# Optimization experiments

Hardware: AMD Instinct MI355X
Metric: run time of the kernel (lower is better)

Reference implementation:

```python
import jax, jax.numpy as jnp
import numpy as np

EPS = 1e-12  # layer_norm_eps

def _ln(h, g, b):
    m = jnp.mean(h, axis=-1, keepdims=True)
    v = jnp.var(h, axis=-1, keepdims=True)
    return (h - m) / jnp.sqrt(v + EPS) * g + b

def setup_inputs() -> dict:
    key = jax.random.key(0)
    B, L, C, N = 32, 512, 256, 16
    ks = jax.random.split(key, 8)
    f = jax.random.normal
    return {
        'query': f(ks[0], (B, L, C), jnp.float32),
        'x': f(ks[1], (B, L, C), jnp.float32),
        'offset': f(ks[2], (B, L, 2 * N), jnp.float32) * 0.1,
        'w1': f(ks[3], (L, L // 4), jnp.float32) * 0.02, 'b1': jnp.zeros((L // 4,), jnp.float32),
        'g1': jnp.ones((L // 4,), jnp.float32), 'bt1': jnp.zeros((L // 4,), jnp.float32),
        'w2': f(ks[4], (L // 4, L), jnp.float32) * 0.02, 'b2': jnp.zeros((L,), jnp.float32),
        'w3': f(ks[5], (C, C), jnp.float32) * 0.02, 'b3': jnp.zeros((C,), jnp.float32),
        'g3': jnp.ones((C,), jnp.float32), 'bt3': jnp.zeros((C,), jnp.float32),
        'w4': f(ks[6], (C, 2 * N), jnp.float32) * 0.02, 'b4': jnp.zeros((2 * N,), jnp.float32),
    }

def reference(query, x, offset, w1, b1, g1, bt1, w2, b2, w3, b3, g3, bt3, w4, b4):
    B, L, C = x.shape
    N = w4.shape[1] // 2
    # sample_layer: Linear over the sequence axis (query permuted to [B,C,L])
    q = jnp.swapaxes(query, 1, 2)                                        # [B,C,L]
    q = jax.nn.gelu(_ln(q @ w1 + b1, g1, bt1), approximate=False) @ w2 + b2
    q = jnp.swapaxes(q, 1, 2)                                            # [B,L,C]
    # adjust_layer over channels -> per-step 2N offsets, tanh * 0.02
    adj = jax.nn.gelu(_ln(q @ w3 + b3, g3, bt3), approximate=False) @ w4 + b4
    adj = jnp.tanh(adj) * 0.02                                           # [B,L,2N]
    local = (offset + adj).reshape(B, L, N, 2)
    # precomputed reference points (x-coord 0, y-coord depends on query step i)
    i = jnp.arange(L, dtype=x.dtype)
    n = jnp.arange(N, dtype=x.dtype) + 0.5
    ref_y = n[None, :] * 2.0 * (i[:, None] + 1e-9) / (N * L) - 1.0       # [L,N]
    ref = jnp.stack([jnp.zeros_like(ref_y), ref_y], axis=-1)             # [L,N,2]
    pos = jnp.tanh(local + ref[None])                                    # [B,L,N,2]
    # grid_sample equivalent: input [B*L, C, H=L, W=1], align_corners=True,
    # bilinear, zero padding. With W=1 the x-coordinate always maps to col 0,
    # so only pos[...,1] matters. Causal mask zeroes keys h > query step l
    # before sampling; since bilinear sampling is linear in the input, we mask
    # the two gathered taps instead of materializing the O(B*L*L*C) tensor.
    pix = (pos[..., 1] + 1.0) * 0.5 * (L - 1)                            # [B,L,N]
    i0f = jnp.floor(pix)
    frac = pix - i0f
    i0 = i0f.astype(jnp.int32)
    i1 = i0 + 1
    lpos = jnp.arange(L, dtype=jnp.int32)[None, :, None]
    v0 = (i0 >= 0) & (i0 < L) & (i0 <= lpos)
    v1 = (i1 >= 0) & (i1 < L) & (i1 <= lpos)
    c0 = jnp.clip(i0, 0, L - 1)
    c1 = jnp.clip(i1, 0, L - 1)
    bidx = jnp.arange(B)[:, None, None]
    val0 = x[bidx, c0]                                                   # [B,L,N,C]
    val1 = x[bidx, c1]                                                   # [B,L,N,C]
    w0 = jnp.where(v0, 1.0 - frac, 0.0)
    w1_ = jnp.where(v1, frac, 0.0)
    out = w0[..., None] * val0 + w1_[..., None] * val1                   # [B,L,N,C]
    return (out, offset, pos)
```

## Files before the change

kernel.cpp:

```cpp
#include <hip/hip_runtime.h>
#include <hip/hip_fp16.h>
#include <math.h>


typedef _Float16 f16;
typedef _Float16 f16x8 __attribute__((ext_vector_type(8)));
typedef float f32x4 __attribute__((ext_vector_type(4)));

#define ZERO4 f32x4{0.f, 0.f, 0.f, 0.f}

__device__ __forceinline__ float gelu_exact(float v) {
  return 0.5f * v * (1.0f + erff(v * 0.70710678118654752f));
}

__global__ __launch_bounds__(256) void k0_prep(
    const float* __restrict__ w1, const float* __restrict__ w2,
    const float* __restrict__ w3, const float* __restrict__ w4,
    f16* __restrict__ w1T, f16* __restrict__ w2T,
    f16* __restrict__ w3T, f16* __restrict__ w4T) {
  __shared__ f16 tile[64][80];
  int blk = blockIdx.x;
  const int tid = threadIdx.x;
  const float* in; f16* out; int R, Cc, tr, tc;
  if (blk < 16)      { in = w1; out = w1T; R = 512; Cc = 128; tr = blk >> 1; tc = blk & 1; }
  else if (blk < 32) { blk -= 16; in = w2; out = w2T; R = 128; Cc = 512; tr = blk >> 3; tc = blk & 7; }
  else if (blk < 48) { blk -= 32; in = w3; out = w3T; R = 256; Cc = 256; tr = blk >> 2; tc = blk & 3; }
  else               { blk -= 48; in = w4; out = w4T; R = 256; Cc = 32;  tr = blk;      tc = 0; }
  const int r0 = tr * 64, c0 = tc * 64;
  for (int id = tid; id < 4096; id += 256) {
    int rr = id >> 6, cc = id & 63;
    if (c0 + cc < Cc) tile[cc][rr] = (f16)in[(r0 + rr) * Cc + c0 + cc];
  }
  __syncthreads();
  for (int id = tid; id < 512; id += 256) {
    int cc = id >> 3, ch = id & 7;
    if (c0 + cc < Cc)
      *(f16x8*)(out + (c0 + cc) * R + r0 + ch * 8) = *(f16x8*)&tile[cc][ch * 8];
  }
}

__global__ __launch_bounds__(256) void k12_sample(
    const float* __restrict__ query, const f16* __restrict__ w1T,
    const f16* __restrict__ w2T,
    const float* __restrict__ b1, const float* __restrict__ g1,
    const float* __restrict__ bt1, const float* __restrict__ b2,
    f16* __restrict__ qout) {
  __shared__ char pool[38912];
  const int tid = threadIdx.x;
  const int b = blockIdx.x >> 4;
  const int c0 = (blockIdx.x & 15) << 4;
  const int lane = tid & 63, w = tid >> 6;
  const int mrow = lane & 15, kg = lane >> 4;
  char* At = pool;
  char* Bt = pool + 2048;
  char* t1s = pool + 32768;
  float* sb2 = (float*)(pool + 36864);

  sb2[tid] = b2[tid];
  sb2[tid + 256] = b2[tid + 256];

  const int qll = tid >> 4, qcc = tid & 15;
  const int wrj = tid >> 3, wch = tid & 7;
  float qv[4]; f16x8 wv[4];
#pragma unroll
  for (int it = 0; it < 4; ++it) {
    qv[it] = query[(((b << 9) + qll + it * 16) << 8) + c0 + qcc];
    wv[it] = *(const f16x8*)(w1T + (wrj + it * 32) * 512 + wch * 8);
  }

  f32x4 acc[2] = {ZERO4, ZERO4};
  for (int s = 0; s < 8; ++s) {
#pragma unroll
    for (int it = 0; it < 4; ++it) {
      int ll = qll + it * 16;
      *(f16*)(At + qcc * 128 + ((2 * ll) ^ ((qcc & 7) << 4))) = (f16)qv[it];
    }
#pragma unroll
    for (int it = 0; it < 4; ++it) {
      int rj = wrj + it * 32;
      *(f16x8*)(Bt + rj * 128 + ((wch * 16) ^ ((rj & 7) << 4))) = wv[it];
    }
    __syncthreads();
    if (s < 7) {
      const int k0n = (s + 1) << 6;
#pragma unroll
      for (int it = 0; it < 4; ++it) {
        qv[it] = query[(((b << 9) + k0n + qll + it * 16) << 8) + c0 + qcc];
        wv[it] = *(const f16x8*)(w1T + (wrj + it * 32) * 512 + k0n + wch * 8);
      }
    }
#pragma unroll
    for (int kk = 0; kk < 2; ++kk) {
      f16x8 a = *(const f16x8*)(At + mrow * 128 + (((kk << 6) + (kg << 4)) ^ ((mrow & 7) << 4)));
#pragma unroll
      for (int nf = 0; nf < 2; ++nf) {
        int rn = w * 32 + nf * 16 + mrow;
        f16x8 bfr = *(const f16x8*)(Bt + rn * 128 + (((kk << 6) + (kg << 4)) ^ ((rn & 7) << 4)));
        acc[nf] = __builtin_amdgcn_mfma_f32_16x16x32_f16(a, bfr, acc[nf], 0, 0, 0);
      }
    }
    __syncthreads();
  }

  f16x8 av[8];
#pragma unroll
  for (int it = 0; it < 8; ++it)
    av[it] = *(const f16x8*)(w2T + ((tid >> 4) + it * 16) * 128 + (tid & 15) * 8);

  float (*hs)[132] = (float(*)[132])pool;
#pragma unroll
  for (int nf = 0; nf < 2; ++nf)
#pragma unroll
    for (int i = 0; i < 4; ++i)
      hs[kg * 4 + i][w * 32 + nf * 16 + mrow] = acc[nf][i];
  __syncthreads();
  {
    const int r = tid >> 4, g = tid & 15;
    float s1 = 0.f, s2 = 0.f, vals[8];
#pragma unroll
    for (int jj = 0; jj < 8; ++jj) {
      int j = g * 8 + jj;
      float v = hs[r][j] + b1[j];
      vals[jj] = v; s1 += v; s2 += v * v;
    }
#pragma unroll
    for (int m = 1; m < 16; m <<= 1) { s1 += __shfl_xor(s1, m, 64); s2 += __shfl_xor(s2, m, 64); }
    const float mean = s1 * (1.f / 128.f);
    float var = fmaxf(s2 * (1.f / 128.f) - mean * mean, 0.f);
    const float rstd = rsqrtf(var + 1e-12f);
    f16 ov[8];
#pragma unroll
    for (int jj = 0; jj < 8; ++jj) {
      int j = g * 8 + jj;
      float v = (vals[jj] - mean) * rstd * g1[j] + bt1[j];
      ov[jj] = (f16)gelu_exact(v);
    }
    __syncthreads();
    *(f16x8*)(t1s + r * 256 + ((g * 16) ^ ((r & 7) << 4))) = *(f16x8*)ov;
  }
  __syncthreads();

  char* At2 = pool;
  const int ar2 = tid >> 4, ac2 = tid & 15;
  for (int lc = 0; lc < 4; ++lc) {
#pragma unroll
    for (int it = 0; it < 8; ++it) {
      int r = ar2 + it * 16;
      *(f16x8*)(At2 + r * 256 + ((ac2 * 16) ^ ((r & 7) << 4))) = av[it];
    }
    __syncthreads();
    if (lc < 3) {
#pragma unroll
      for (int it = 0; it < 8; ++it)
        av[it] = *(const f16x8*)(w2T + ((lc + 1) * 128 + ar2 + it * 16) * 128 + ac2 * 8);
    }
    f32x4 acc2[2] = {ZERO4, ZERO4};
#pragma unroll
    for (int ks = 0; ks < 4; ++ks) {
      f16x8 bfr = *(const f16x8*)(t1s + mrow * 256 + (((ks << 6) + (kg << 4)) ^ ((mrow & 7) << 4)));
#pragma unroll
      for (int mf = 0; mf < 2; ++mf) {
        int rm = w * 32 + mf * 16 + mrow;
        f16x8 a = *(const f16x8*)(At2 + rm * 256 + (((ks << 6) + (kg << 4)) ^ ((rm & 7) << 4)));
        acc2[mf] = __builtin_amdgcn_mfma_f32_16x16x32_f16(a, bfr, acc2[mf], 0, 0, 0);
      }
    }
#pragma unroll
    for (int mf = 0; mf < 2; ++mf)
#pragma unroll
      for (int i = 0; i < 4; ++i) {
        int l = lc * 128 + w * 32 + mf * 16 + kg * 4 + i;
        qout[((b << 9) + l) * 256 + c0 + mrow] = (f16)(acc2[mf][i] + sb2[l]);
      }
    __syncthreads();
  }
}

__global__ __launch_bounds__(256) void k3_adjust(
    const f16* __restrict__ qbuf, const f16* __restrict__ w3T,
    const float* __restrict__ b3, const float* __restrict__ g3,
    const float* __restrict__ bt3, const f16* __restrict__ w4T,
    const float* __restrict__ b4, const float* __restrict__ offset,
    float* __restrict__ off_out, float* __restrict__ pos_out) {
  __shared__ char pool[34816];
  __shared__ char w4t[32 * 512];
  __shared__ float sb3[256];
  const int tid = threadIdx.x;
  const int b = blockIdx.x >> 5;
  const int l0 = (blockIdx.x & 31) << 4;
  const int lane = tid & 63, w = tid >> 6;
  const int mrow = lane & 15, kg = lane >> 4;
  char* At = pool;
  char* Bt = pool + 2048;

  for (int id = tid; id < 1024; id += 256) {
    int r = id >> 5, c = id & 31;
    f16x8 v = *(const f16x8*)(w4T + r * 256 + c * 8);
    *(f16x8*)(w4t + r * 512 + ((c * 16) ^ ((r & 7) << 4))) = v;
  }
  sb3[tid] = b3[tid];

  const int sr = tid >> 3, sc = tid & 7;
  f16x8 aq; f16x8 bq[8];
  if (tid < 128) aq = *(const f16x8*)(qbuf + ((b << 9) + l0 + sr) * 256 + sc * 8);
#pragma unroll
  for (int it = 0; it < 8; ++it)
    bq[it] = *(const f16x8*)(w3T + (sr + it * 32) * 256 + sc * 8);

  f32x4 acc[4] = {ZERO4, ZERO4, ZERO4, ZERO4};
  for (int s = 0; s < 4; ++s) {
    if (tid < 128)
      *(f16x8*)(At + sr * 128 + ((sc * 16) ^ ((sr & 7) << 4))) = aq;
#pragma unroll
    for (int it = 0; it < 8; ++it) {
      int r = sr + it * 32;
      *(f16x8*)(Bt + r * 128 + ((sc * 16) ^ ((r & 7) << 4))) = bq[it];
    }
    __syncthreads();
    if (s < 3) {
      const int k0n = (s + 1) << 6;
      if (tid < 128) aq = *(const f16x8*)(qbuf + ((b << 9) + l0 + sr) * 256 + k0n + sc * 8);
#pragma unroll
      for (int it = 0; it < 8; ++it)
        bq[it] = *(const f16x8*)(w3T + (sr + it * 32) * 256 + k0n + sc * 8);
    }
#pragma unroll
    for (int kk = 0; kk < 2; ++kk) {
      f16x8 a = *(const f16x8*)(At + mrow * 128 + (((kk << 6) + (kg << 4)) ^ ((mrow & 7) << 4)));
#pragma unroll
      for (int nf = 0; nf < 4; ++nf) {
        int rn = w * 64 + nf * 16 + mrow;
        f16x8 bfr = *(const f16x8*)(Bt + rn * 128 + (((kk << 6) + (kg << 4)) ^ ((rn & 7) << 4)));
        acc[nf] = __builtin_amdgcn_mfma_f32_16x16x32_f16(a, bfr, acc[nf], 0, 0, 0);
      }
    }
    __syncthreads();
  }
  float (*hs)[264] = (float(*)[264])pool;
  char* ts = pool + 17408;
#pragma unroll
  for (int nf = 0; nf < 4; ++nf) {
    int col = w * 64 + nf * 16 + mrow;
    float bias = sb3[col];
#pragma unroll
    for (int i = 0; i < 4; ++i)
      hs[kg * 4 + i][col] = acc[nf][i] + bias;
  }
  __syncthreads();
  {
    const int r = tid >> 4, g = tid & 15;
    float s1 = 0.f, s2 = 0.f, vals[16];
#pragma unroll
    for (int jj = 0; jj < 16; ++jj) {
      float v = hs[r][g * 16 + jj];
      vals[jj] = v; s1 += v; s2 += v * v;
    }
#pragma unroll
    for (int m = 1; m < 16; m <<= 1) { s1 += __shfl_xor(s1, m, 64); s2 += __shfl_xor(s2, m, 64); }
    const float mean = s1 * (1.f / 256.f);
    float var = fmaxf(s2 * (1.f / 256.f) - mean * mean, 0.f);
    const float rstd = rsqrtf(var + 1e-12f);
    f16 ov[16];
#pragma unroll
    for (int jj = 0; jj < 16; ++jj) {
      int kch = g * 16 + jj;
      float v = (vals[jj] - mean) * rstd * g3[kch] + bt3[kch];
      ov[jj] = (f16)gelu_exact(v);
    }
    *(f16x8*)(ts + r * 512 + ((g * 32) ^ ((r & 7) << 4))) = *(f16x8*)&ov[0];
    *(f16x8*)(ts + r * 512 + ((g * 32 + 16) ^ ((r & 7) << 4))) = *(f16x8*)&ov[8];
  }
  __syncthreads();
  if (w < 2) {
    const int n4 = w;
    f32x4 a4 = ZERO4;
#pragma unroll
    for (int ks = 0; ks < 8; ++ks) {
      f16x8 a = *(const f16x8*)(ts + mrow * 512 + (((ks << 6) + (kg << 4)) ^ ((mrow & 7) << 4)));
      int br = n4 * 16 + mrow;
      f16x8 bb = *(const f16x8*)(w4t + br * 512 + (((ks << 6) + (kg << 4)) ^ ((br & 7) << 4)));
      a4 = __builtin_amdgcn_mfma_f32_16x16x32_f16(a, bb, a4, 0, 0, 0);
    }
    const int col = n4 * 16 + mrow;
#pragma unroll
    for (int i = 0; i < 4; ++i) {
      const int row = kg * 4 + i;
      const int l = l0 + row;
      float adj = tanhf(a4[i] + b4[col]) * 0.02f;
      float padj = __shfl_xor(adj, 1, 64);
      if ((lane & 1) == 0) {
        const int n = col >> 1;
        const float2 offv = *(const float2*)(offset + (((b << 9) + l) << 5) + col);
        const float pos0v = tanhf(offv.x + adj);
        const float ref_y = ((float)n + 0.5f) * ((float)l + 1e-9f) * (1.0f / 4096.0f) - 1.0f;
        const float pos1v = tanhf(offv.y + padj + ref_y);
        *(float2*)(off_out + (((b << 9) + l) << 5) + col) = offv;
        *(float2*)(pos_out + (((b << 9) + l) << 5) + col) = make_float2(pos0v, pos1v);
      }
    }
  }
}

__global__ __launch_bounds__(256) void k4_gather(
    const float* __restrict__ x, const float* __restrict__ pos,
    float* __restrict__ outbuf) {
  const int blk = blockIdx.x;
  const int b = ((blk & 7) << 2) | ((blk >> 3) & 3);
  const int grp = blk >> 5;
  const int w = threadIdx.x >> 6, lane = threadIdx.x & 63;
  const int p0 = (grp << 5) + (w << 3);
  const unsigned tbase = ((unsigned)b << 13) + (unsigned)p0;
  const f32x4* xb = (const f32x4*)x + ((unsigned)(b << 9)) * 64u + lane;
  f32x4* ob = (f32x4*)outbuf + (unsigned)tbase * 64u + lane;

  float pw[8];
#pragma unroll
  for (int i = 0; i < 8; ++i) pw[i] = pos[(tbase + i) * 2 + 1];

  int cc0[8], cc1[8];
  float w0v[8], w1v[8];
#pragma unroll
  for (int i = 0; i < 8; ++i) {
    const int l = (p0 + i) >> 4;
    const float pix = (pw[i] + 1.0f) * 0.5f * 511.0f;
    const float i0f = floorf(pix);
    const int i0 = (int)i0f;
    const float frac = pix - i0f;
    const int i1 = i0 + 1;
    const bool v0 = (i0 >= 0) && (i0 < 512) && (i0 <= l);
    const bool v1 = (i1 >= 0) && (i1 < 512) && (i1 <= l);
    cc0[i] = i0 < 0 ? 0 : (i0 > 511 ? 511 : i0);
    cc1[i] = i1 < 0 ? 0 : (i1 > 511 ? 511 : i1);
    w0v[i] = v0 ? (1.0f - frac) : 0.0f;
    w1v[i] = v1 ? frac : 0.0f;
  }

#pragma unroll
  for (int g = 0; g < 2; ++g) {
    f32x4 va[4], vb[4];
#pragma unroll
    for (int j = 0; j < 4; ++j) {
      va[j] = xb[(unsigned)cc0[g * 4 + j] * 64u];
      vb[j] = xb[(unsigned)cc1[g * 4 + j] * 64u];
    }
#pragma unroll
    for (int j = 0; j < 4; ++j) {
      f32x4 o = w0v[g * 4 + j] * va[j] + w1v[g * 4 + j] * vb[j];
      __builtin_nontemporal_store(o, ob + (unsigned)(g * 4 + j) * 64u);
    }
  }
}

extern "C" void kernel_launch(void* const* d_in, const int* in_sizes, int n_in,
                              void* d_out, int out_size, void* d_ws, size_t ws_size,
                              hipStream_t stream) {
  const float* query  = (const float*)d_in[0];
  const float* x      = (const float*)d_in[1];
  const float* offset = (const float*)d_in[2];
  const float* w1  = (const float*)d_in[3];
  const float* b1  = (const float*)d_in[4];
  const float* g1  = (const float*)d_in[5];
  const float* bt1 = (const float*)d_in[6];
  const float* w2  = (const float*)d_in[7];
  const float* b2  = (const float*)d_in[8];
  const float* w3  = (const float*)d_in[9];
  const float* b3  = (const float*)d_in[10];
  const float* g3  = (const float*)d_in[11];
  const float* bt3 = (const float*)d_in[12];
  const float* w4  = (const float*)d_in[13];
  const float* b4  = (const float*)d_in[14];

  float* out     = (float*)d_out;
  float* off_out = out + 67108864;
  float* pos_out = off_out + 524288;

  f16* w1T = (f16*)d_ws;
  f16* w2T = w1T + 65536;
  f16* w3T = w2T + 65536;
  f16* w4T = w3T + 65536;
  f16* q   = w4T + 8192;

  k0_prep<<<52, 256, 0, stream>>>(w1, w2, w3, w4, w1T, w2T, w3T, w4T);
  k12_sample<<<512, 256, 0, stream>>>(query, w1T, w2T, b1, g1, bt1, b2, q);
  k3_adjust<<<1024, 256, 0, stream>>>(q, w3T, b3, g3, bt3, w4T, b4, offset,
                                      off_out, pos_out);
  k4_gather<<<8192, 256, 0, stream>>>(x, pos_out, out);
}
```

Measured before the change: 109.1 us.

## Split fused sample kernel into split-K GEMM1, LayerNorm, and tiled GEMM2 kernels

Replaces the single fused sample-layer kernel with three kernels: a split-K first GEMM over four K-chunks writing fp32 partials (2048 blocks), a reduction+LayerNorm+GELU kernel producing an fp16 intermediate, and a larger-tile second GEMM with 64-column output tiles. The aim is more parallelism and better occupancy than the earlier 512-block serial-K fused kernel. It also drops the LDS staging of w4 and b3 in the adjust kernel, reading them directly from global memory. In exchange it adds global round trips for the partials and intermediate, plus two extra launches.

```diff
diff --git a/kernel.cpp b/kernel.cpp
--- a/kernel.cpp
+++ b/kernel.cpp
@@ -39,37 +39,32 @@
   }
 }
 
-__global__ __launch_bounds__(256) void k12_sample(
+__global__ __launch_bounds__(256) void k1_gemm1(
     const float* __restrict__ query, const f16* __restrict__ w1T,
-    const f16* __restrict__ w2T,
-    const float* __restrict__ b1, const float* __restrict__ g1,
-    const float* __restrict__ bt1, const float* __restrict__ b2,
-    f16* __restrict__ qout) {
-  __shared__ char pool[38912];
+    float* __restrict__ hpart) {
+  __shared__ __align__(16) char pool[18432];
   const int tid = threadIdx.x;
-  const int b = blockIdx.x >> 4;
-  const int c0 = (blockIdx.x & 15) << 4;
+  const int b = blockIdx.x >> 6;
+  const int c0 = ((blockIdx.x >> 2) & 15) << 4;
+  const int ks = blockIdx.x & 3;
   const int lane = tid & 63, w = tid >> 6;
   const int mrow = lane & 15, kg = lane >> 4;
   char* At = pool;
   char* Bt = pool + 2048;
-  char* t1s = pool + 32768;
-  float* sb2 = (float*)(pool + 36864);
-
-  sb2[tid] = b2[tid];
-  sb2[tid + 256] = b2[tid + 256];
 
   const int qll = tid >> 4, qcc = tid & 15;
   const int wrj = tid >> 3, wch = tid & 7;
+  const int kbase = ks << 7;
+
   float qv[4]; f16x8 wv[4];
 #pragma unroll
   for (int it = 0; it < 4; ++it) {
-    qv[it] = query[(((b << 9) + qll + it * 16) << 8) + c0 + qcc];
-    wv[it] = *(const f16x8*)(w1T + (wrj + it * 32) * 512 + wch * 8);
+    qv[it] = query[(((b << 9) + kbase + qll + it * 16) << 8) + c0 + qcc];
+    wv[it] = *(const f16x8*)(w1T + (wrj + it * 32) * 512 + kbase + wch * 8);
   }
 
   f32x4 acc[2] = {ZERO4, ZERO4};
-  for (int s = 0; s < 8; ++s) {
+  for (int s = 0; s < 2; ++s) {
 #pragma unroll
     for (int it = 0; it < 4; ++it) {
       int ll = qll + it * 16;
@@ -81,8 +76,8 @@
       *(f16x8*)(Bt + rj * 128 + ((wch * 16) ^ ((rj & 7) << 4))) = wv[it];
     }
     __syncthreads();
-    if (s < 7) {
-      const int k0n = (s + 1) << 6;
+    if (s == 0) {
+      const int k0n = kbase + 64;
 #pragma unroll
       for (int it = 0; it < 4; ++it) {
         qv[it] = query[(((b << 9) + k0n + qll + it * 16) << 8) + c0 + qcc];
@@ -101,79 +96,109 @@
     }
     __syncthreads();
   }
-
-  f16x8 av[8];
-#pragma unroll
-  for (int it = 0; it < 8; ++it)
-    av[it] = *(const f16x8*)(w2T + ((tid >> 4) + it * 16) * 128 + (tid & 15) * 8);
-
-  float (*hs)[132] = (float(*)[132])pool;
+  const unsigned hb = ((unsigned)ks << 20) + ((unsigned)b << 15);
 #pragma unroll
   for (int nf = 0; nf < 2; ++nf)
 #pragma unroll
     for (int i = 0; i < 4; ++i)
-      hs[kg * 4 + i][w * 32 + nf * 16 + mrow] = acc[nf][i];
+      hpart[hb + ((unsigned)(c0 + kg * 4 + i) << 7) + (unsigned)(w * 32 + nf * 16 + mrow)] = acc[nf][i];
+}
+
+__global__ __launch_bounds__(256) void k2a_ln(
+    const float* __restrict__ hpart, const float* __restrict__ b1,
+    const float* __restrict__ g1, const float* __restrict__ bt1,
+    f16* __restrict__ t1) {
+  const int tid = threadIdx.x;
+  const int row = blockIdx.x * 16 + (tid >> 4);
+  const int g = tid & 15;
+  const int j0 = g * 8;
+  const unsigned base = ((unsigned)row << 7) + (unsigned)j0;
+
+  float a8[8] = {0.f, 0.f, 0.f, 0.f, 0.f, 0.f, 0.f, 0.f};
+#pragma unroll
+  for (int ks = 0; ks < 4; ++ks) {
+    const float* p = hpart + ((unsigned)ks << 20) + base;
+    f32x4 u0 = *(const f32x4*)p;
+    f32x4 u1 = *(const f32x4*)(p + 4);
+    a8[0] += u0.x; a8[1] += u0.y; a8[2] += u0.z; a8[3] += u0.w;
+    a8[4] += u1.x; a8[5] += u1.y; a8[6] += u1.z; a8[7] += u1.w;
+  }
+  float vals[8], s1 = 0.f, s2 = 0.f;
+#pragma unroll
+  for (int jj = 0; jj < 8; ++jj) {
+    float v = a8[jj] + b1[j0 + jj];
+    vals[jj] = v; s1 += v; s2 += v * v;
+  }
+#pragma unroll
+  for (int m = 1; m < 16; m <<= 1) { s1 += __shfl_xor(s1, m, 64); s2 += __shfl_xor(s2, m, 64); }
+  const float mean = s1 * (1.f / 128.f);
+  float var = fmaxf(s2 * (1.f / 128.f) - mean * mean, 0.f);
+  const float rstd = rsqrtf(var + 1e-12f);
+  f16 ov[8];
+#pragma unroll
+  for (int jj = 0; jj < 8; ++jj) {
+    float v = (vals[jj] - mean) * rstd * g1[j0 + jj] + bt1[j0 + jj];
+    ov[jj] = (f16)gelu_exact(v);
+  }
+  *(f16x8*)(t1 + base) = *(f16x8*)ov;
+}
+
+__global__ __launch_bounds__(256) void k2b_gemm2(
+    const f16* __restrict__ w2T, const f16* __restrict__ t1,
+    const float* __restrict__ b2, f16* __restrict__ qout) {
+  __shared__ __align__(16) char pool[49152];
+  const int tid = threadIdx.x;
+  const int b = blockIdx.x >> 4;
+  const int l0 = ((blockIdx.x >> 2) & 3) << 7;
+  const int c0 = (blockIdx.x & 3) << 6;
+  const int lane = tid & 63, w = tid >> 6;
+  const int mrow = lane & 15, kg = lane >> 4;
+  char* At2 = pool;
+  char* Bt2 = pool + 32768;
+
+  const int r16 = tid >> 4, cch = tid & 15;
+#pragma unroll
+  for (int it = 0; it < 8; ++it) {
+    int r = r16 + it * 16;
+    f16x8 v = *(const f16x8*)(w2T + (l0 + r) * 128 + cch * 8);
+    *(f16x8*)(At2 + r * 256 + ((cch * 16) ^ ((r & 7) << 4))) = v;
+  }
+#pragma unroll
+  for (int it = 0; it < 4; ++it) {
+    int r = r16 + it * 16;
+    f16x8 v = *(const f16x8*)(t1 + ((b << 8) + c0 + r) * 128 + cch * 8);
+    *(f16x8*)(Bt2 + r * 256 + ((cch * 16) ^ ((r & 7) << 4))) = v;
+  }
   __syncthreads();
-  {
-    const int r = tid >> 4, g = tid & 15;
-    float s1 = 0.f, s2 = 0.f, vals[8];
-#pragma unroll
-    for (int jj = 0; jj < 8; ++jj) {
-      int j = g * 8 + jj;
-      float v = hs[r][j] + b1[j];
-      vals[jj] = v; s1 += v; s2 += v * v;
-    }
-#pragma unroll
-    for (int m = 1; m < 16; m <<= 1) { s1 += __shfl_xor(s1, m, 64); s2 += __shfl_xor(s2, m, 64); }
-    const float mean = s1 * (1.f / 128.f);
-    float var = fmaxf(s2 * (1.f / 128.f) - mean * mean, 0.f);
-    const float rstd = rsqrtf(var + 1e-12f);
-    f16 ov[8];
-#pragma unroll
-    for (int jj = 0; jj < 8; ++jj) {
-      int j = g * 8 + jj;
-      float v = (vals[jj] - mean) * rstd * g1[j] + bt1[j];
-      ov[jj] = (f16)gelu_exact(v);
-    }
-    __syncthreads();
-    *(f16x8*)(t1s + r * 256 + ((g * 16) ^ ((r & 7) << 4))) = *(f16x8*)ov;
-  }
-  __syncthreads();
-
-  char* At2 = pool;
-  const int ar2 = tid >> 4, ac2 = tid & 15;
-  for (int lc = 0; lc < 4; ++lc) {
-#pragma unroll
-    for (int it = 0; it < 8; ++it) {
-      int r = ar2 + it * 16;
-      *(f16x8*)(At2 + r * 256 + ((ac2 * 16) ^ ((r & 7) << 4))) = av[it];
-    }
-    __syncthreads();
-    if (lc < 3) {
-#pragma unroll
-      for (int it = 0; it < 8; ++it)
-        av[it] = *(const f16x8*)(w2T + ((lc + 1) * 128 + ar2 + it * 16) * 128 + ac2 * 8);
-    }
-    f32x4 acc2[2] = {ZERO4, ZERO4};
-#pragma unroll
-    for (int ks = 0; ks < 4; ++ks) {
-      f16x8 bfr = *(const f16x8*)(t1s + mrow * 256 + (((ks << 6) + (kg << 4)) ^ ((mrow & 7) << 4)));
-#pragma unroll
-      for (int mf = 0; mf < 2; ++mf) {
-        int rm = w * 32 + mf * 16 + mrow;
-        f16x8 a = *(const f16x8*)(At2 + rm * 256 + (((ks << 6) + (kg << 4)) ^ ((rm & 7) << 4)));
-        acc2[mf] = __builtin_amdgcn_mfma_f32_16x16x32_f16(a, bfr, acc2[mf], 0, 0, 0);
-      }
-    }
-#pragma unroll
-    for (int mf = 0; mf < 2; ++mf)
-#pragma unroll
-      for (int i = 0; i < 4; ++i) {
-        int l = lc * 128 + w * 32 + mf * 16 + kg * 4 + i;
-        qout[((b << 9) + l) * 256 + c0 + mrow] = (f16)(acc2[mf][i] + sb2[l]);
-      }
-    __syncthreads();
-  }
+
+  f32x4 acc[2][4] = {{ZERO4, ZERO4, ZERO4, ZERO4}, {ZERO4, ZERO4, ZERO4, ZERO4}};
+#pragma unroll
+  for (int ks = 0; ks < 4; ++ks) {
+    f16x8 a[2];
+#pragma unroll
+    for (int mf = 0; mf < 2; ++mf) {
+      int rm = w * 32 + mf * 16 + mrow;
+      a[mf] = *(const f16x8*)(At2 + rm * 256 + (((ks << 6) + (kg << 4)) ^ ((rm & 7) << 4)));
+    }
+#pragma unroll
+    for (int nf = 0; nf < 4; ++nf) {
+      int rn = nf * 16 + mrow;
+      f16x8 bfr = *(const f16x8*)(Bt2 + rn * 256 + (((ks << 6) + (kg << 4)) ^ ((rn & 7) << 4)));
+#pragma unroll
+      for (int mf = 0; mf < 2; ++mf)
+        acc[mf][nf] = __builtin_amdgcn_mfma_f32_16x16x32_f16(a[mf], bfr, acc[mf][nf], 0, 0, 0);
+    }
+  }
+#pragma unroll
+  for (int mf = 0; mf < 2; ++mf)
+#pragma unroll
+    for (int i = 0; i < 4; ++i) {
+      int l = l0 + w * 32 + mf * 16 + kg * 4 + i;
+      float bb2 = b2[l];
+#pragma unroll
+      for (int nf = 0; nf < 4; ++nf)
+        qout[((b << 9) + l) * 256 + c0 + nf * 16 + mrow] = (f16)(acc[mf][nf][i] + bb2);
+    }
 }
 
 __global__ __launch_bounds__(256) void k3_adjust(
@@ -182,9 +207,7 @@
     const float* __restrict__ bt3, const f16* __restrict__ w4T,
     const float* __restrict__ b4, const float* __restrict__ offset,
     float* __restrict__ off_out, float* __restrict__ pos_out) {
-  __shared__ char pool[34816];
-  __shared__ char w4t[32 * 512];
-  __shared__ float sb3[256];
+  __shared__ __align__(16) char pool[34816];
   const int tid = threadIdx.x;
   const int b = blockIdx.x >> 5;
   const int l0 = (blockIdx.x & 31) << 4;
@@ -193,13 +216,6 @@
   char* At = pool;
   char* Bt = pool + 2048;
 
-  for (int id = tid; id < 1024; id += 256) {
-    int r = id >> 5, c = id & 31;
-    f16x8 v = *(const f16x8*)(w4T + r * 256 + c * 8);
-    *(f16x8*)(w4t + r * 512 + ((c * 16) ^ ((r & 7) << 4))) = v;
-  }
-  sb3[tid] = b3[tid];
-
   const int sr = tid >> 3, sc = tid & 7;
   f16x8 aq; f16x8 bq[8];
   if (tid < 128) aq = *(const f16x8*)(qbuf + ((b << 9) + l0 + sr) * 256 + sc * 8);
@@ -241,7 +257,7 @@
 #pragma unroll
   for (int nf = 0; nf < 4; ++nf) {
     int col = w * 64 + nf * 16 + mrow;
-    float bias = sb3[col];
+    float bias = b3[col];
 #pragma unroll
     for (int i = 0; i < 4; ++i)
       hs[kg * 4 + i][col] = acc[nf][i] + bias;
@@ -278,7 +294,7 @@
     for (int ks = 0; ks < 8; ++ks) {
       f16x8 a = *(const f16x8*)(ts + mrow * 512 + (((ks << 6) + (kg << 4)) ^ ((mrow & 7) << 4)));
       int br = n4 * 16 + mrow;
-      f16x8 bb = *(const f16x8*)(w4t + br * 512 + (((ks << 6) + (kg << 4)) ^ ((br & 7) << 4)));
+      f16x8 bb = *(const f16x8*)(w4T + br * 256 + ks * 32 + kg * 8);
       a4 = __builtin_amdgcn_mfma_f32_16x16x32_f16(a, bb, a4, 0, 0, 0);
     }
     const int col = n4 * 16 + mrow;
@@ -378,10 +394,14 @@
   f16* w2T = w1T + 65536;
   f16* w3T = w2T + 65536;
   f16* w4T = w3T + 65536;
-  f16* q   = w4T + 8192;
+  f16* t1  = w4T + 8192;
+  float* hpart = (float*)(t1 + 1048576);
+  f16* q = (f16*)hpart;
 
   k0_prep<<<52, 256, 0, stream>>>(w1, w2, w3, w4, w1T, w2T, w3T, w4T);
-  k12_sample<<<512, 256, 0, stream>>>(query, w1T, w2T, b1, g1, bt1, b2, q);
+  k1_gemm1<<<2048, 256, 0, stream>>>(query, w1T, hpart);
+  k2a_ln<<<512, 256, 0, stream>>>(hpart, b1, g1, bt1, t1);
+  k2b_gemm2<<<512, 256, 0, stream>>>(w2T, t1, b2, q);
   k3_adjust<<<1024, 256, 0, stream>>>(q, w3T, b3, g3, bt3, w4T, b4, offset,
                                       off_out, pos_out);
   k4_gather<<<8192, 256, 0, stream>>>(x, pos_out, out);
```

After: 110.3 us. About the same (+1.1%).
